# Performance work log

Hardware: AMD Instinct MI355X
Metric: run time of the kernel (lower is better)

Reference implementation:

```python
import jax, jax.numpy as jnp
import numpy as np

B, S, D_MODEL = 8, 1024, 512
DIM_K = DIM_V = 512
N_HEADS = 8
DK = DIM_K // N_HEADS
DV = DIM_V // N_HEADS
NORM = 1.0 / np.sqrt(D_MODEL).astype(np.float32)  # note: 1/sqrt(d_model), per source


def setup_inputs() -> dict:
    key = jax.random.key(0)
    ks = jax.random.split(key, 6)
    s = 0.05  # small init to keep softmax well-conditioned
    return {
        "x": jax.random.normal(ks[0], (B, S, D_MODEL), jnp.float32),
        "y": jax.random.normal(ks[1], (B, S, D_MODEL), jnp.float32),
        "q_w": jax.random.normal(ks[2], (D_MODEL, DIM_K), jnp.float32) * s,
        "q_b": jnp.zeros((DIM_K,), jnp.float32),
        "k_w": jax.random.normal(ks[3], (D_MODEL, DIM_K), jnp.float32) * s,
        "k_b": jnp.zeros((DIM_K,), jnp.float32),
        "v_w": jax.random.normal(ks[4], (D_MODEL, DIM_V), jnp.float32) * s,
        "v_b": jnp.zeros((DIM_V,), jnp.float32),
        "o_w": jax.random.normal(ks[5], (DIM_V, D_MODEL), jnp.float32) * s,
        "o_b": jnp.zeros((D_MODEL,), jnp.float32),
    }


def reference(x, y, q_w, q_b, k_w, k_b, v_w, v_b, o_w, o_b):
    b, s, _ = x.shape
    # Faithful to torch: plain row-major reshape (B,S,dim) -> (H,B,S,dh),
    # NOT a per-token head split.
    Q = (x @ q_w + q_b).reshape(N_HEADS, b, s, DK)
    K = (y @ k_w + k_b).reshape(N_HEADS, b, s, DK)
    V = (y @ v_w + v_b).reshape(N_HEADS, b, s, DV)
    scores = jnp.einsum("hbqd,hbkd->hbqk", Q, K) * NORM  # [H,B,S,S]
    # dynamic mean-threshold mask: keep only scores strictly above row mean
    thre = jnp.mean(scores, axis=-1, keepdims=True)
    scores = jnp.where(scores > thre, scores, -jnp.inf)
    attn = jax.nn.softmax(scores, axis=-1)
    out = jnp.einsum("hbqk,hbkd->hbqd", attn, V).reshape(b, s, DIM_V)
    return out @ o_w + o_b
```

## Files before the change

### kernel.cpp

```cpp
#include <hip/hip_runtime.h>
#include <hip/hip_bf16.h>
#include <hip/hip_fp16.h>


typedef _Float16 f16;
typedef __attribute__((ext_vector_type(4))) _Float16 f16x4;
typedef __attribute__((ext_vector_type(8))) _Float16 f16x8;
typedef __attribute__((ext_vector_type(8))) short bf16x8;
typedef __attribute__((ext_vector_type(4))) float f32x4;

#define MFMA16(a, b, c) __builtin_amdgcn_mfma_f32_16x16x32_f16((a), (b), (c), 0, 0, 0)
#define MFMAB16(a, b, c) __builtin_amdgcn_mfma_f32_16x16x32_bf16((a), (b), (c), 0, 0, 0)
#define MFMAPV(a, b, c) __builtin_amdgcn_mfma_f32_16x16x16f16((a), (b), (c), 0, 0, 0)

#if defined(__has_builtin) && __has_builtin(__builtin_amdgcn_exp2f)
#define EXPFN(x) __builtin_amdgcn_exp2f(x)
#define QPROJ_SCALE (0.04419417382415922f * 1.4426950408889634f)
#else
#define EXPFN(x) __expf(x)
#define QPROJ_SCALE 0.04419417382415922f
#endif

#define GLL16(gp, lp)                                       \
  __builtin_amdgcn_global_load_lds(                         \
      (const __attribute__((address_space(1))) void*)(gp),  \
      (__attribute__((address_space(3))) void*)(lp), 16, 0, 0)

__device__ __forceinline__ float b2f(short s) {
  return __uint_as_float(((unsigned)(unsigned short)s) << 16);
}

__device__ __forceinline__ void splitbf(float v, short& h, short& l) {
  unsigned short hu = __bfloat16_as_ushort(__float2bfloat16(v));
  h = (short)hu;
  float hf = __uint_as_float(((unsigned)hu) << 16);
  l = (short)__bfloat16_as_ushort(__float2bfloat16(v - hf));
}

__global__ __launch_bounds__(256) void k_pre(
    const float* __restrict__ x, const float* __restrict__ y,
    const float* __restrict__ qw, const float* __restrict__ kw,
    const float* __restrict__ vw, const float* __restrict__ ow,
    short* __restrict__ qh, short* __restrict__ ql, short* __restrict__ kh,
    short* __restrict__ kl, f16* __restrict__ vt, f16* __restrict__ ot,
    short* __restrict__ Xh, short* __restrict__ Xl, short* __restrict__ Yh,
    short* __restrict__ Yl, f16* __restrict__ Ym) {
  const int tid = threadIdx.x;
  const int bx = blockIdx.x;
  const int by = blockIdx.y;
  if (bx < 512) {
    const int wt = by * 512 + bx;
    const int z = wt >> 8;
    const int tile = wt & 255;
    const int bxx = tile & 15, byy = tile >> 4;
    const float* W = (z == 0) ? qw : (z == 1) ? kw : (z == 2) ? vw : ow;
    __shared__ float t[32][33];
    const int tx = tid & 31, ty = tid >> 5;
#pragma unroll
    for (int i = 0; i < 32; i += 8)
      t[ty + i][tx] = W[(size_t)(byy * 32 + ty + i) * 512 + bxx * 32 + tx];
    __syncthreads();
#pragma unroll
    for (int i = 0; i < 32; i += 8) {
      size_t idx = (size_t)(bxx * 32 + ty + i) * 512 + byy * 32 + tx;
      float v = t[tx][ty + i];
      if (z < 2) {
        short h, l;
        splitbf(v, h, l);
        if (z == 0) { qh[idx] = h; ql[idx] = l; }
        else { kh[idx] = h; kl[idx] = l; }
      } else {
        if (z == 2) vt[idx] = (f16)v;
        else ot[idx] = (f16)v;
      }
    }
  }
  const float* src = by ? y : x;
  short* dh = by ? Yh : Xh;
  short* dl = by ? Yl : Xl;
  const size_t i = ((size_t)bx * 256 + tid) * 8;
  float4 a = *(const float4*)(src + i);
  float4 b = *(const float4*)(src + i + 4);
  float v[8] = {a.x, a.y, a.z, a.w, b.x, b.y, b.z, b.w};
  bf16x8 h, l;
#pragma unroll
  for (int j = 0; j < 8; ++j) {
    short hh, ll;
    splitbf(v[j], hh, ll);
    h[j] = hh;
    l[j] = ll;
  }
  *(bf16x8*)(dh + i) = h;
  *(bf16x8*)(dl + i) = l;
  if (by) {
    f16x8 m8;
#pragma unroll
    for (int j = 0; j < 8; ++j) m8[j] = (f16)v[j];
    *(f16x8*)(Ym + i) = m8;
  }
}

#define GSTAGE(buf, kk)                                              \
  {                                                                  \
    _Pragma("unroll") for (int j = 0; j < 4; ++j) {                  \
      const int rowu = half + j * 16;                                \
      const int row = rowu + srow;                                   \
      const int slog = sslot ^ ((row >> 1) & 3);                     \
      GLL16(gsb + (size_t)(rb + row) * 512 + (kk) + slog * 8,        \
            &ldsb[buf][rowu][0]);                                    \
    }                                                                \
  }

template <typename OT>
__device__ __forceinline__ void gemm16_gll(const f16* __restrict__ A,
                                           const f16* __restrict__ WT,
                                           const float* __restrict__ bias,
                                           OT* __restrict__ C, int m0, int n0,
                                           f16 (*As)[128][32],
                                           f16 (*Bs)[128][32]) {
  const int tid = threadIdx.x;
  const int wv = tid >> 6, lane = tid & 63;
  const int wm = wv >> 1, wn = wv & 1;
  const int l15 = lane & 15, lg = lane >> 4;
  const int srow = lane >> 2, sslot = lane & 3;

  const f16* gsb = (wv < 2) ? A : WT;
  const int rb = (wv < 2) ? m0 : n0;
  f16(*ldsb)[128][32] = (wv < 2) ? As : Bs;
  const int half = (wv & 1) * 64;

  const f32x4 fz = {0.f, 0.f, 0.f, 0.f};
  f32x4 acc[4][4];
#pragma unroll
  for (int m = 0; m < 4; ++m)
#pragma unroll
    for (int n = 0; n < 4; ++n) acc[m][n] = fz;

  GSTAGE(0, 0);
  int cur = 0;
  for (int k0 = 0; k0 < 512; k0 += 32) {
    __syncthreads();
    if (k0 < 480) GSTAGE(cur ^ 1, k0 + 32);
    f16x8 af[4], bf[4];
#pragma unroll
    for (int m = 0; m < 4; ++m) {
      const int r = wm * 64 + m * 16 + l15;
      af[m] = *(const f16x8*)&As[cur][r][(lg ^ ((r >> 1) & 3)) * 8];
    }
#pragma unroll
    for (int n = 0; n < 4; ++n) {
      const int r = wn * 64 + n * 16 + l15;
      bf[n] = *(const f16x8*)&Bs[cur][r][(lg ^ ((r >> 1) & 3)) * 8];
    }
#pragma unroll
    for (int m = 0; m < 4; ++m)
#pragma unroll
      for (int n = 0; n < 4; ++n) acc[m][n] = MFMA16(af[m], bf[n], acc[m][n]);
    cur ^= 1;
  }
#pragma unroll
  for (int n = 0; n < 4; ++n) {
    const int col = n0 + wn * 64 + n * 16 + l15;
    const float b = bias[col];
#pragma unroll
    for (int m = 0; m < 4; ++m) {
      const int row = m0 + wm * 64 + m * 16 + lg * 4;
#pragma unroll
      for (int r = 0; r < 4; ++r)
        C[(size_t)(row + r) * 512 + col] = (OT)(acc[m][n][r] + b);
    }
  }
}

#define OSTAGE(buf, kk)                                                       \
  {                                                                           \
    if (wv < 2) {                                                             \
      _Pragma("unroll") for (int j = 0; j < 4; ++j) {                         \
        const int rowu = wv * 64 + j * 16;                                    \
        const int row = rowu + srow;                                          \
        const int slog = sslot ^ ((row >> 1) & 3);                            \
        GLL16(Om + (size_t)(m0 + row) * 512 + (kk) + slog * 8,                \
              &As[buf][rowu][0]);                                             \
      }                                                                       \
    } else {                                                                  \
      _Pragma("unroll") for (int j = 0; j < 2; ++j) {                         \
        const int rowu = (wv - 2) * 32 + j * 16;                              \
        const int row = rowu + srow;                                          \
        const int slog = sslot ^ ((row >> 1) & 3);                            \
        GLL16(owT + (size_t)(n0 + row) * 512 + (kk) + slog * 8,               \
              &Bs[buf][rowu][0]);                                             \
      }                                                                       \
    }                                                                         \
  }

__global__ __launch_bounds__(256) void k_gemm_out(const f16* __restrict__ Om,
                                                  const f16* __restrict__ owT,
                                                  const float* __restrict__ ob,
                                                  float* __restrict__ out) {
  __shared__ __align__(16) f16 As[2][128][32];
  __shared__ __align__(16) f16 Bs[2][64][32];
  const int lid = blockIdx.x + (blockIdx.y << 3);
  const int swz = ((lid & 7) << 6) + (lid >> 3);
  const int m0 = (swz >> 3) * 128, n0 = (swz & 7) * 64;
  const int tid = threadIdx.x;
  const int wv = tid >> 6, lane = tid & 63;
  const int wm = wv >> 1, wn = wv & 1;
  const int l15 = lane & 15, lg = lane >> 4;
  const int srow = lane >> 2, sslot = lane & 3;

  const f32x4 fz = {0.f, 0.f, 0.f, 0.f};
  f32x4 acc[4][2];
#pragma unroll
  for (int m = 0; m < 4; ++m)
#pragma unroll
    for (int n = 0; n < 2; ++n) acc[m][n] = fz;

  OSTAGE(0, 0);
  int cur = 0;
  for (int k0 = 0; k0 < 512; k0 += 32) {
    __syncthreads();
    if (k0 < 480) OSTAGE(cur ^ 1, k0 + 32);
    f16x8 af[4], bf[2];
#pragma unroll
    for (int m = 0; m < 4; ++m) {
      const int r = wm * 64 + m * 16 + l15;
      af[m] = *(const f16x8*)&As[cur][r][(lg ^ ((r >> 1) & 3)) * 8];
    }
#pragma unroll
    for (int n = 0; n < 2; ++n) {
      const int r = wn * 32 + n * 16 + l15;
      bf[n] = *(const f16x8*)&Bs[cur][r][(lg ^ ((r >> 1) & 3)) * 8];
    }
#pragma unroll
    for (int m = 0; m < 4; ++m)
#pragma unroll
      for (int n = 0; n < 2; ++n) acc[m][n] = MFMA16(af[m], bf[n], acc[m][n]);
    cur ^= 1;
  }
#pragma unroll
  for (int n = 0; n < 2; ++n) {
    const int col = n0 + wn * 32 + n * 16 + l15;
    const float b = ob[col];
#pragma unroll
    for (int m = 0; m < 4; ++m) {
      const int row = m0 + wm * 64 + m * 16 + lg * 4;
#pragma unroll
      for (int r = 0; r < 4; ++r)
        out[(size_t)(row + r) * 512 + col] = acc[m][n][r] + b;
    }
  }
}

#define PSTAGE(buf, kk)                                             \
  {                                                                 \
    _Pragma("unroll") for (int j = 0; j < 8; ++j) {                 \
      const int row = j * 16 + srow;                                \
      const int slog = sslot ^ ((row >> 1) & 3);                    \
      GLL16(gsb + (size_t)(rb + row) * 512 + (kk) + slog * 8,       \
            &sm4[buf][wv][j * 16][0]);                              \
    }                                                               \
  }

__global__ __launch_bounds__(256) void k_proj(
    const short* __restrict__ Xh, const short* __restrict__ Xl,
    const short* __restrict__ Yh, const short* __restrict__ Yl,
    const f16* __restrict__ Ym, const short* __restrict__ qwh,
    const short* __restrict__ qwl, const short* __restrict__ kwh,
    const short* __restrict__ kwl, const f16* __restrict__ vwT,
    const float* __restrict__ qb, const float* __restrict__ kbias,
    const float* __restrict__ vb, short* __restrict__ Qh,
    short* __restrict__ Ql, short* __restrict__ Kh, short* __restrict__ Kl,
    f16* __restrict__ Vm, float* __restrict__ Kpart) {
  __shared__ __align__(16) short sm4[2][4][128][32];
  const int lid = blockIdx.x + (blockIdx.y << 2);
  const int swz = ((lid & 7) << 5) + (lid >> 3);
  const int nt = swz & 3, mt = swz >> 2;
  const int m0 = mt * 128, n0 = nt * 128;
  const int z = blockIdx.z;
  if (z == 2) {
    gemm16_gll<f16>(Ym, vwT, vb, Vm, m0, n0, (f16(*)[128][32]) & sm4[0][0][0][0],
                    (f16(*)[128][32]) & sm4[0][2][0][0]);
    return;
  }
  const short* Agh = z ? Yh : Xh;
  const short* Agl = z ? Yl : Xl;
  const short* Wh = z ? kwh : qwh;
  const short* Wl = z ? kwl : qwl;
  const float* bias = z ? kbias : qb;
  short* Ch = z ? Kh : Qh;
  short* Cl = z ? Kl : Ql;
  const float osc = z ? 1.f : (float)QPROJ_SCALE;

  const int tid = threadIdx.x;
  const int wv = tid >> 6, lane = tid & 63;
  const int wm = wv >> 1, wn = wv & 1;
  const int l15 = lane & 15, lg = lane >> 4;
  const int srow = lane >> 2, sslot = lane & 3;

  const short* gsb = (wv == 0) ? Agh : (wv == 1) ? Agl : (wv == 2) ? Wh : Wl;
  const int rb = (wv < 2) ? m0 : n0;

  const f32x4 fz = {0.f, 0.f, 0.f, 0.f};
  f32x4 acc[4][4];
#pragma unroll
  for (int m = 0; m < 4; ++m)
#pragma unroll
    for (int n = 0; n < 4; ++n) acc[m][n] = fz;

  PSTAGE(0, 0);
  int cur = 0;
  for (int k0 = 0; k0 < 512; k0 += 32) {
    __syncthreads();
    if (k0 < 480) PSTAGE(cur ^ 1, k0 + 32);
    bf16x8 afh[4], afl[4], bfh[4], bfl[4];
#pragma unroll
    for (int m = 0; m < 4; ++m) {
      const int r = wm * 64 + m * 16 + l15;
      const int sl = (lg ^ ((r >> 1) & 3)) * 8;
      afh[m] = *(const bf16x8*)&sm4[cur][0][r][sl];
      afl[m] = *(const bf16x8*)&sm4[cur][1][r][sl];
    }
#pragma unroll
    for (int n = 0; n < 4; ++n) {
      const int r = wn * 64 + n * 16 + l15;
      const int sl = (lg ^ ((r >> 1) & 3)) * 8;
      bfh[n] = *(const bf16x8*)&sm4[cur][2][r][sl];
      bfl[n] = *(const bf16x8*)&sm4[cur][3][r][sl];
    }
#pragma unroll
    for (int m = 0; m < 4; ++m)
#pragma unroll
      for (int n = 0; n < 4; ++n) {
        acc[m][n] = MFMAB16(afh[m], bfh[n], acc[m][n]);
        acc[m][n] = MFMAB16(afh[m], bfl[n], acc[m][n]);
        acc[m][n] = MFMAB16(afl[m], bfh[n], acc[m][n]);
      }
    cur ^= 1;
  }
  float csum[4];
#pragma unroll
  for (int n = 0; n < 4; ++n) {
    const int col = n0 + wn * 64 + n * 16 + l15;
    const float b = bias[col];
    csum[n] = 16.f * b;
#pragma unroll
    for (int m = 0; m < 4; ++m) {
      const int row = m0 + wm * 64 + m * 16 + lg * 4;
#pragma unroll
      for (int r = 0; r < 4; ++r) {
        const float vraw = acc[m][n][r] + b;
        csum[n] += acc[m][n][r];
        short h, l;
        splitbf(vraw * osc, h, l);
        const size_t idx = (size_t)(row + r) * 512 + col;
        Ch[idx] = h;
        Cl[idx] = l;
      }
    }
  }
  if (z == 1) {
    float* cred = (float*)&sm4[0][0][0][0];
    __syncthreads();
#pragma unroll
    for (int n = 0; n < 4; ++n)
      cred[(wn * 64 + n * 16 + l15) * 8 + wm * 4 + lg] = csum[n];
    __syncthreads();
    if (tid < 64) {
      float s = 0.f;
#pragma unroll
      for (int j = 0; j < 8; ++j)
        s += cred[tid * 8 + j] + cred[(tid + 64) * 8 + j];
      Kpart[((size_t)mt * 4 + nt) * 64 + tid] = s;
    }
  }
}

__global__ __launch_bounds__(256) void k_vtr(const f16* __restrict__ Vm,
                                             f16* __restrict__ Vt) {
  const int p = blockIdx.y;
  const int j0 = blockIdx.x * 16;
  __shared__ f16 L[16][520];
  const int tid = threadIdx.x;
#pragma unroll
  for (int it = 0; it < 4; ++it) {
    int idx = it * 256 + tid;
    int row = idx >> 6, oct = idx & 63;
    *(f16x8*)&L[row][oct * 8] =
        *(const f16x8*)&Vm[(size_t)(p * 128 + j0 + row) * 512 + oct * 8];
  }
  __syncthreads();
#pragma unroll
  for (int it = 0; it < 4; ++it) {
    int idx = it * 256 + tid;
    int dh = idx >> 4, j = idx & 15;
    f16x8 v;
#pragma unroll
    for (int g = 0; g < 8; ++g) v[g] = L[j][g * 64 + dh];
    *(f16x8*)&Vt[((size_t)p * 64 + dh) * 1024 + (j0 + j) * 8] = v;
  }
}

#define STAGE(b, cc)                                       \
  {                                                        \
    GLL16(KhSrc + (cc) * 4096, &KhS[b][skey][slot8 * 8]);  \
    GLL16(KlSrc + (cc) * 4096, &KlS[b][skey][slot8 * 8]);  \
    GLL16(VSrc + (cc) * 64, &Vs[b][skey][slot8 * 8]);      \
  }

#define CHUNK(cb_, c_)                                                        \
  {                                                                           \
    __syncthreads();       \
    if ((c_) < 15) STAGE((cb_) ^ 1, (c_) + 1);       \
    __builtin_amdgcn_s_setprio(1);                                            \
    f32x4 aa[4];                                                              \
    _Pragma("unroll") for (int t = 0; t < 4; ++t) {                           \
      const int krow = t * 16 + l15;                                          \
      const int ksw = l15 & 7;                           \
      bf16x8 kh0 = *(const bf16x8*)&KhS[cb_][krow][(lg ^ ksw) * 8];           \
      bf16x8 kh1 = *(const bf16x8*)&KhS[cb_][krow][((4 + lg) ^ ksw) * 8];     \
      bf16x8 kl0 = *(const bf16x8*)&KlS[cb_][krow][(lg ^ ksw) * 8];           \
      bf16x8 kl1 = *(const bf16x8*)&KlS[cb_][krow][((4 + lg) ^ ksw) * 8];     \
      f32x4 s1 = fz, s2 = fz;                                                 \
      s1 = MFMAB16(kh0, qh0, s1);                                             \
      s2 = MFMAB16(kh1, qh1, s2);                                             \
      s1 = MFMAB16(kl0, qh0, s1);                                             \
      s2 = MFMAB16(kl1, qh1, s2);                                             \
      s1 = MFMAB16(kh0, ql0, s1);                                             \
      s2 = MFMAB16(kh1, ql1, s2);                                             \
      aa[t] = s1 + s2;                                                        \
    }                                                                         \
    f16x4 va[4][4];                                                           \
    _Pragma("unroll") for (int d0 = 0; d0 < 4; ++d0) {                        \
      const int vrow = d0 * 16 + l15;                                         \
      const int vsw = l15 & 7;                                                \
      _Pragma("unroll") for (int t = 0; t < 4; ++t)                           \
        va[d0][t] = *(const f16x4*)&Vs[cb_][vrow]                             \
                        [(((t * 2 + (lg >> 1)) ^ vsw) * 8) + (lg & 1) * 4];   \
    }                                                                         \
    f16x4 pf[4];                                                              \
    _Pragma("unroll") for (int t = 0; t < 4; ++t)                             \
      _Pragma("unroll") for (int r = 0; r < 4; ++r) {                         \
        float v = aa[t][r];                                                   \
        pf[t][r] = (f16)((v > sm) ? EXPFN(v) : 0.f);                          \
      }                                                                       \
    _Pragma("unroll") for (int t = 0; t < 4; ++t) {                           \
      od = MFMAPV(kones, pf[t], od);                                          \
      _Pragma("unroll") for (int d0 = 0; d0 < 4; ++d0)                        \
        oac[d0] = MFMAPV(va[d0][t], pf[t], oac[d0]);                          \
    }                                                                         \
    __builtin_amdgcn_s_setprio(0);                                            \
  }

__global__ __launch_bounds__(512, 4) void k_attn(
    const short* __restrict__ Qh, const short* __restrict__ Ql,
    const short* __restrict__ Kh, const short* __restrict__ Kl,
    const f16* __restrict__ Vt, const float* __restrict__ Kpart,
    f16* __restrict__ Om) {
  constexpr int S = 1024, DH = 64;
  const int p = blockIdx.x;
  const int qt = blockIdx.y;
  const size_t pb = (size_t)p * S * DH;
  const short* Qhp = Qh + pb;
  const short* Qlp = Ql + pb;
  const short* Khp = Kh + pb;
  const short* Klp = Kl + pb;
  const f16* Vtp = Vt + pb;
  f16* Op = Om + pb;

  const int tid = threadIdx.x;
  const int w = tid >> 6, lane = tid & 63;
  const int l15 = lane & 15, lg = lane >> 4;

  __shared__ __align__(16) short KhS[2][64][64];
  __shared__ __align__(16) short KlS[2][64][64];
  __shared__ __align__(16) f16 Vs[2][64][64];

  const int skey = tid >> 3;
  const int slot8 = tid & 7;
  const int ssw = skey & 7;
  const short* KhSrc = Khp + skey * 64 + (slot8 ^ ssw) * 8;
  const short* KlSrc = Klp + skey * 64 + (slot8 ^ ssw) * 8;
  const f16* VSrc = Vtp + (size_t)skey * 1024 + (slot8 ^ ssw) * 8;

  STAGE(0, 0);

  const int qrow = qt * 128 + w * 16;
  const size_t qo = (size_t)(qrow + l15) * DH + lg * 8;
  bf16x8 qh0 = *(const bf16x8*)(Qhp + qo);
  bf16x8 ql0 = *(const bf16x8*)(Qlp + qo);
  bf16x8 qh1 = *(const bf16x8*)(Qhp + qo + 32);
  bf16x8 ql1 = *(const bf16x8*)(Qlp + qo + 32);

  const float* kp = Kpart + (size_t)p * 256;
  float km0[8], km1[8];
#pragma unroll
  for (int j = 0; j < 8; ++j) { km0[j] = 0.f; km1[j] = 0.f; }
#pragma unroll
  for (int pt = 0; pt < 4; ++pt) {
    const float* bb = kp + pt * 64;
#pragma unroll
    for (int j = 0; j < 8; ++j) {
      km0[j] += bb[lg * 8 + j];
      km1[j] += bb[32 + lg * 8 + j];
    }
  }
  float sm = 0.f;
#pragma unroll
  for (int j = 0; j < 8; ++j) {
    sm += (b2f(qh0[j]) + b2f(ql0[j])) * km0[j] +
          (b2f(qh1[j]) + b2f(ql1[j])) * km1[j];
  }
  sm += __shfl_xor(sm, 16);
  sm += __shfl_xor(sm, 32);
  sm *= (1.f / 1024.f);

  const f32x4 fz = {0.f, 0.f, 0.f, 0.f};
  const f16x4 kones = {(f16)1.f, (f16)1.f, (f16)1.f, (f16)1.f};
  f32x4 oac[4];
#pragma unroll
  for (int d = 0; d < 4; ++d) oac[d] = fz;
  f32x4 od = fz;

  for (int cc = 0; cc < 16; cc += 2) {
    CHUNK(0, cc);
    CHUNK(1, cc + 1);
  }

  const float inv = 1.f / od[0];
#pragma unroll
  for (int d0 = 0; d0 < 4; ++d0) {
    f16x4 o0;
#pragma unroll
    for (int r = 0; r < 4; ++r) o0[r] = (f16)(oac[d0][r] * inv);
    *(f16x4*)&Op[(size_t)(qrow + l15) * DH + d0 * 16 + lg * 4] = o0;
  }
}

extern "C" void kernel_launch(void* const* d_in, const int* in_sizes, int n_in,
                              void* d_out, int out_size, void* d_ws,
                              size_t ws_size, hipStream_t stream) {
  const float* x = (const float*)d_in[0];
  const float* y = (const float*)d_in[1];
  const float* qw = (const float*)d_in[2];
  const float* qb = (const float*)d_in[3];
  const float* kw = (const float*)d_in[4];
  const float* kbias = (const float*)d_in[5];
  const float* vw = (const float*)d_in[6];
  const float* vb = (const float*)d_in[7];
  const float* ow = (const float*)d_in[8];
  const float* ob = (const float*)d_in[9];
  float* out = (float*)d_out;

  char* ws = (char*)d_ws;
  const size_t WT_B = 512ull * 512 * 2;
  const size_t MAT_B = 8192ull * 512 * 2;
  short* qwhT = (short*)(ws + 0 * WT_B);
  short* qwlT = (short*)(ws + 1 * WT_B);
  short* kwhT = (short*)(ws + 2 * WT_B);
  short* kwlT = (short*)(ws + 3 * WT_B);
  f16* vwT = (f16*)(ws + 4 * WT_B);
  f16* owT = (f16*)(ws + 5 * WT_B);
  char* m = ws + 6 * WT_B;
  short* Qh = (short*)(m + 0 * MAT_B);
  short* Ql = (short*)(m + 1 * MAT_B);
  short* Kh = (short*)(m + 2 * MAT_B);
  short* Kl = (short*)(m + 3 * MAT_B);
  f16* Vm = (f16*)(m + 4 * MAT_B);
  short* Xh = (short*)(m + 5 * MAT_B);
  short* Xl = (short*)(m + 6 * MAT_B);
  short* Yh = (short*)(m + 7 * MAT_B);
  short* Yl = (short*)(m + 8 * MAT_B);
  f16* Ym = (f16*)(m + 9 * MAT_B);
  float* Kpart = (float*)(m + 10 * MAT_B);
  f16* Vtr = (f16*)Xh;
  f16* Om = (f16*)Yh;

  hipLaunchKernelGGL(k_pre, dim3(2048, 2), dim3(256), 0, stream, x, y, qw, kw,
                     vw, ow, qwhT, qwlT, kwhT, kwlT, vwT, owT, Xh, Xl, Yh, Yl,
                     Ym);
  hipLaunchKernelGGL(k_proj, dim3(4, 64, 3), dim3(256), 0, stream, Xh, Xl, Yh,
                     Yl, Ym, qwhT, qwlT, kwhT, kwlT, vwT, qb, kbias, vb, Qh,
                     Ql, Kh, Kl, Vm, Kpart);
  hipLaunchKernelGGL(k_vtr, dim3(8, 64), dim3(256), 0, stream, Vm, Vtr);
  hipLaunchKernelGGL(k_attn, dim3(64, 8), dim3(512), 0, stream, Qh, Ql, Kh,
                     Kl, Vtr, Kpart, Om);
  hipLaunchKernelGGL(k_gemm_out, dim3(8, 64), dim3(256), 0, stream, Om, owT,
                     ob, out);
}
```

Measured before the change: 116.1 us.

## Split attention key chunks across wave pairs, each wave owning two query tiles

Each wave now handles two 16-row query tiles but only half of every 64-key chunk. Waves 0-3 and 4-7 split the keys and merge their partial outputs and denominators through shared memory at the end. This reuses each K/V fragment read from LDS for two query tiles, halving LDS reads per MFMA. In exchange, register pressure rises (two accumulator sets, eight Q fragments) and a final cross-wave reduction with extra barriers is added.

```diff
diff --git a/kernel.cpp b/kernel.cpp
--- a/kernel.cpp
+++ b/kernel.cpp
@@ -412,41 +412,44 @@
     __syncthreads();       \
     if ((c_) < 15) STAGE((cb_) ^ 1, (c_) + 1);       \
     __builtin_amdgcn_s_setprio(1);                                            \
-    f32x4 aa[4];                                                              \
-    _Pragma("unroll") for (int t = 0; t < 4; ++t) {                           \
+    _Pragma("unroll") for (int th = 0; th < 2; ++th) {                        \
+      const int t = tbase + th;                                               \
       const int krow = t * 16 + l15;                                          \
       const int ksw = l15 & 7;                           \
       bf16x8 kh0 = *(const bf16x8*)&KhS[cb_][krow][(lg ^ ksw) * 8];           \
       bf16x8 kh1 = *(const bf16x8*)&KhS[cb_][krow][((4 + lg) ^ ksw) * 8];     \
       bf16x8 kl0 = *(const bf16x8*)&KlS[cb_][krow][(lg ^ ksw) * 8];           \
       bf16x8 kl1 = *(const bf16x8*)&KlS[cb_][krow][((4 + lg) ^ ksw) * 8];     \
-      f32x4 s1 = fz, s2 = fz;                                                 \
-      s1 = MFMAB16(kh0, qh0, s1);                                             \
-      s2 = MFMAB16(kh1, qh1, s2);                                             \
-      s1 = MFMAB16(kl0, qh0, s1);                                             \
-      s2 = MFMAB16(kl1, qh1, s2);                                             \
-      s1 = MFMAB16(kh0, ql0, s1);                                             \
-      s2 = MFMAB16(kh1, ql1, s2);                                             \
-      aa[t] = s1 + s2;                                                        \
-    }                                                                         \
-    f16x4 va[4][4];                                                           \
-    _Pragma("unroll") for (int d0 = 0; d0 < 4; ++d0) {                        \
-      const int vrow = d0 * 16 + l15;                                         \
-      const int vsw = l15 & 7;                                                \
-      _Pragma("unroll") for (int t = 0; t < 4; ++t)                           \
-        va[d0][t] = *(const f16x4*)&Vs[cb_][vrow]                             \
-                        [(((t * 2 + (lg >> 1)) ^ vsw) * 8) + (lg & 1) * 4];   \
-    }                                                                         \
-    f16x4 pf[4];                                                              \
-    _Pragma("unroll") for (int t = 0; t < 4; ++t)                             \
+      f32x4 a0 = fz, a1 = fz;          \
+      a0 = MFMAB16(kh0, q0h0, a0);                                            \
+      a1 = MFMAB16(kh0, q1h0, a1);                                            \
+      a0 = MFMAB16(kh1, q0h1, a0);                                            \
+      a1 = MFMAB16(kh1, q1h1, a1);                                            \
+      a0 = MFMAB16(kl0, q0h0, a0);                                            \
+      a1 = MFMAB16(kl0, q1h0, a1);                                            \
+      a0 = MFMAB16(kh0, q0l0, a0);                                            \
+      a1 = MFMAB16(kh0, q1l0, a1);                                            \
+      a0 = MFMAB16(kl1, q0h1, a0);                                            \
+      a1 = MFMAB16(kl1, q1h1, a1);                                            \
+      a0 = MFMAB16(kh1, q0l1, a0);                                            \
+      a1 = MFMAB16(kh1, q1l1, a1);                                            \
+      f16x4 pf0, pf1;                                                         \
       _Pragma("unroll") for (int r = 0; r < 4; ++r) {                         \
-        float v = aa[t][r];                                                   \
-        pf[t][r] = (f16)((v > sm) ? EXPFN(v) : 0.f);                          \
+        float v0 = a0[r];                                                     \
+        pf0[r] = (f16)((v0 > sm0) ? EXPFN(v0) : 0.f);                         \
+        float v1 = a1[r];                                                     \
+        pf1[r] = (f16)((v1 > sm1) ? EXPFN(v1) : 0.f);                         \
       }                                                                       \
-    _Pragma("unroll") for (int t = 0; t < 4; ++t) {                           \
-      od = MFMAPV(kones, pf[t], od);                                          \
-      _Pragma("unroll") for (int d0 = 0; d0 < 4; ++d0)                        \
-        oac[d0] = MFMAPV(va[d0][t], pf[t], oac[d0]);                          \
+      od0 = MFMAPV(kones, pf0, od0);                                          \
+      od1 = MFMAPV(kones, pf1, od1);                                          \
+      _Pragma("unroll") for (int d0 = 0; d0 < 4; ++d0) {                      \
+        const int vrow = d0 * 16 + l15;                                       \
+        const int vsw = l15 & 7;                                              \
+        f16x4 va = *(const f16x4*)&Vs[cb_][vrow]                              \
+                       [(((t * 2 + (lg >> 1)) ^ vsw) * 8) + (lg & 1) * 4];    \
+        oac0[d0] = MFMAPV(va, pf0, oac0[d0]);                                 \
+        oac1[d0] = MFMAPV(va, pf1, oac1[d0]);                                 \
+      }                                                                       \
     }                                                                         \
     __builtin_amdgcn_s_setprio(0);                                            \
   }
@@ -470,10 +473,13 @@
   const int tid = threadIdx.x;
   const int w = tid >> 6, lane = tid & 63;
   const int l15 = lane & 15, lg = lane >> 4;
-
-  __shared__ __align__(16) short KhS[2][64][64];
-  __shared__ __align__(16) short KlS[2][64][64];
-  __shared__ __align__(16) f16 Vs[2][64][64];
+  const int qg = w & 3;
+  const int tbase = (w >> 2) * 2;
+
+  __shared__ __align__(16) char smem[49152];
+  short(*KhS)[64][64] = (short(*)[64][64])smem;
+  short(*KlS)[64][64] = (short(*)[64][64])(smem + 16384);
+  f16(*Vs)[64][64] = (f16(*)[64][64])(smem + 32768);
 
   const int skey = tid >> 3;
   const int slot8 = tid & 7;
@@ -484,12 +490,17 @@
 
   STAGE(0, 0);
 
-  const int qrow = qt * 128 + w * 16;
-  const size_t qo = (size_t)(qrow + l15) * DH + lg * 8;
-  bf16x8 qh0 = *(const bf16x8*)(Qhp + qo);
-  bf16x8 ql0 = *(const bf16x8*)(Qlp + qo);
-  bf16x8 qh1 = *(const bf16x8*)(Qhp + qo + 32);
-  bf16x8 ql1 = *(const bf16x8*)(Qlp + qo + 32);
+  const int qrow = qt * 128 + qg * 32;
+  const size_t qo0 = (size_t)(qrow + l15) * DH + lg * 8;
+  const size_t qo1 = (size_t)(qrow + 16 + l15) * DH + lg * 8;
+  bf16x8 q0h0 = *(const bf16x8*)(Qhp + qo0);
+  bf16x8 q0l0 = *(const bf16x8*)(Qlp + qo0);
+  bf16x8 q0h1 = *(const bf16x8*)(Qhp + qo0 + 32);
+  bf16x8 q0l1 = *(const bf16x8*)(Qlp + qo0 + 32);
+  bf16x8 q1h0 = *(const bf16x8*)(Qhp + qo1);
+  bf16x8 q1l0 = *(const bf16x8*)(Qlp + qo1);
+  bf16x8 q1h1 = *(const bf16x8*)(Qhp + qo1 + 32);
+  bf16x8 q1l1 = *(const bf16x8*)(Qlp + qo1 + 32);
 
   const float* kp = Kpart + (size_t)p * 256;
   float km0[8], km1[8];
@@ -504,35 +515,61 @@
       km1[j] += bb[32 + lg * 8 + j];
     }
   }
-  float sm = 0.f;
+  float sm0 = 0.f, sm1 = 0.f;
 #pragma unroll
   for (int j = 0; j < 8; ++j) {
-    sm += (b2f(qh0[j]) + b2f(ql0[j])) * km0[j] +
-          (b2f(qh1[j]) + b2f(ql1[j])) * km1[j];
-  }
-  sm += __shfl_xor(sm, 16);
-  sm += __shfl_xor(sm, 32);
-  sm *= (1.f / 1024.f);
+    sm0 += (b2f(q0h0[j]) + b2f(q0l0[j])) * km0[j] +
+           (b2f(q0h1[j]) + b2f(q0l1[j])) * km1[j];
+    sm1 += (b2f(q1h0[j]) + b2f(q1l0[j])) * km0[j] +
+           (b2f(q1h1[j]) + b2f(q1l1[j])) * km1[j];
+  }
+  sm0 += __shfl_xor(sm0, 16); sm0 += __shfl_xor(sm0, 32);
+  sm1 += __shfl_xor(sm1, 16); sm1 += __shfl_xor(sm1, 32);
+  sm0 *= (1.f / 1024.f);
+  sm1 *= (1.f / 1024.f);
 
   const f32x4 fz = {0.f, 0.f, 0.f, 0.f};
   const f16x4 kones = {(f16)1.f, (f16)1.f, (f16)1.f, (f16)1.f};
-  f32x4 oac[4];
-#pragma unroll
-  for (int d = 0; d < 4; ++d) oac[d] = fz;
-  f32x4 od = fz;
+  f32x4 oac0[4], oac1[4];
+#pragma unroll
+  for (int d = 0; d < 4; ++d) { oac0[d] = fz; oac1[d] = fz; }
+  f32x4 od0 = fz, od1 = fz;
 
   for (int cc = 0; cc < 16; cc += 2) {
     CHUNK(0, cc);
     CHUNK(1, cc + 1);
   }
 
-  const float inv = 1.f / od[0];
-#pragma unroll
-  for (int d0 = 0; d0 < 4; ++d0) {
-    f16x4 o0;
-#pragma unroll
-    for (int r = 0; r < 4; ++r) o0[r] = (f16)(oac[d0][r] * inv);
-    *(f16x4*)&Op[(size_t)(qrow + l15) * DH + d0 * 16 + lg * 4] = o0;
+  __syncthreads();
+  float* MRG = (float*)smem;
+  if (w >= 4) {
+    float* dst = MRG + ((size_t)qg * 64 + lane) * 34;
+#pragma unroll
+    for (int d0 = 0; d0 < 4; ++d0)
+#pragma unroll
+      for (int r = 0; r < 4; ++r) {
+        dst[d0 * 4 + r] = oac0[d0][r];
+        dst[16 + d0 * 4 + r] = oac1[d0][r];
+      }
+    dst[32] = od0[0];
+    dst[33] = od1[0];
+  }
+  __syncthreads();
+  if (w < 4) {
+    const float* src = MRG + ((size_t)qg * 64 + lane) * 34;
+    const float inv0 = 1.f / (od0[0] + src[32]);
+    const float inv1 = 1.f / (od1[0] + src[33]);
+#pragma unroll
+    for (int d0 = 0; d0 < 4; ++d0) {
+      f16x4 o0, o1;
+#pragma unroll
+      for (int r = 0; r < 4; ++r) {
+        o0[r] = (f16)((oac0[d0][r] + src[d0 * 4 + r]) * inv0);
+        o1[r] = (f16)((oac1[d0][r] + src[16 + d0 * 4 + r]) * inv1);
+      }
+      *(f16x4*)&Op[(size_t)(qrow + l15) * DH + d0 * 16 + lg * 4] = o0;
+      *(f16x4*)&Op[(size_t)(qrow + 16 + l15) * DH + d0 * 16 + lg * 4] = o1;
+    }
   }
 }
 
```

Measured after the change: 115.4 us, median of 2. About the same (-0.6%).
